# Optimization experiments

Hardware: AMD Instinct MI355X
Metric: run time of the kernel (lower is better)

The kernel has to match this reference:

```python
import jax, jax.numpy as jnp
import numpy as np

EPS = 1e-5

def _conv3x3(x, w, b):
    # NCHW, OIHW, 3x3 stride 1 pad 1
    y = jax.lax.conv_general_dilated(x, w, window_strides=(1, 1),
                                     padding=((1, 1), (1, 1)),
                                     dimension_numbers=('NCHW', 'OIHW', 'NCHW'))
    return y + b[None, :, None, None]

def _pool_upsample(x, k):
    # adaptive avg pool to (H/k, W/k) then nearest block-upsample back
    B, C, H, W = x.shape
    p = x.reshape(B, C, H // k, k, W // k, k).mean(axis=(3, 5))
    return jnp.repeat(jnp.repeat(p, k, axis=2), k, axis=3)

def setup_inputs() -> dict:
    key = jax.random.key(0)
    ks = jax.random.split(key, 12)
    B, C, H, W = 32, 8, 300, 300
    d = {
        'x': jax.random.normal(ks[0], (B, C, H, W), jnp.float32),
        'w5': jax.random.normal(ks[1], (8, 16, 3, 3), jnp.float32) * 0.1,
        'b5': jnp.zeros((8,), jnp.float32),
        'w10': jax.random.normal(ks[2], (8, 16, 3, 3), jnp.float32) * 0.1,
        'b10': jnp.zeros((8,), jnp.float32),
        'w15': jax.random.normal(ks[3], (8, 16, 3, 3), jnp.float32) * 0.1,
        'b15': jnp.zeros((8,), jnp.float32),
        'gw': jax.random.normal(ks[4], (8, 24, 3, 3), jnp.float32) * 0.1,
        'gb': jnp.zeros((8,), jnp.float32),
        'mw': jax.random.normal(ks[5], (8, 24, 3, 3), jnp.float32) * 0.1,
        'mb': jnp.zeros((8,), jnp.float32),
        'gamma': jnp.ones((8,), jnp.float32),
        'beta': jnp.zeros((8,), jnp.float32),
    }
    return d

def reference(x, w5, b5, w10, b10, w15, b15, gw, gb, mw, mb, gamma, beta):
    up5 = _pool_upsample(x, 5)    # [B,8,300,300]
    up10 = _pool_upsample(x, 10)
    up15 = _pool_upsample(x, 15)
    c5 = _conv3x3(jnp.concatenate([x, up5], axis=1), w5, b5)
    c10 = _conv3x3(jnp.concatenate([x, up10], axis=1), w10, b10)
    c15 = _conv3x3(jnp.concatenate([x, up15], axis=1), w15, b15)
    g_in = jnp.concatenate([c5, c10, c15], axis=1)  # [B,24,H,W]
    # gated conv, activation=None: conv(g_in) * sigmoid(mask_conv(g_in))
    y = _conv3x3(g_in, gw, gb) * jax.nn.sigmoid(_conv3x3(g_in, mw, mb))
    # batch norm (training-mode batch stats, biased var, as torch default)
    mean = y.mean(axis=(0, 2, 3), keepdims=True)
    var = ((y - mean) ** 2).mean(axis=(0, 2, 3), keepdims=True)
    y = (y - mean) * jax.lax.rsqrt(var + EPS)
    return y * gamma[None, :, None, None] + beta[None, :, None, None]
```

## Files before the change

### kernel.cpp

```cpp
#include <hip/hip_runtime.h>
#include <math.h>

typedef __bf16 bfrag __attribute__((ext_vector_type(8)));
typedef float f32x4 __attribute__((ext_vector_type(4)));

#define BN 32
#define HH 300
#define WW 300
#define HW 90000
#define NPX (BN * HW)

#define GX 10
#define GY 19

#define P5I_BYTE_OFF   0
#define P10I_BYTE_OFF  1843200
#define P15I_BYTE_OFF  2304000
#define CWB_BYTE_OFF   2508800
#define GWB_BYTE_OFF   2524160
#define STAT_BYTE_OFF  2531328
#define SS_BYTE_OFF    2539520

__device__ __forceinline__ short f2bf(float f) {
    union { float f; unsigned u; } v;
    v.f = f;
    unsigned r = v.u + 0x7FFF + ((v.u >> 16) & 1);
    return (short)(r >> 16);
}

__device__ __forceinline__ float bf2f(unsigned short s) {
    union { unsigned u; float f; } v;
    v.u = ((unsigned)s) << 16;
    return v.f;
}

__global__ void k_setup(const float* __restrict__ w5, const float* __restrict__ w10,
                        const float* __restrict__ w15, const float* __restrict__ gw,
                        const float* __restrict__ mw, short* __restrict__ cBg,
                        short* __restrict__ gBg, double* __restrict__ stats) {
    int t = threadIdx.x;
    for (int idx = t; idx < 7680; idx += 256) {
        int s = idx / 2560, rem = idx % 2560;
        int n = rem / 160, r2 = rem % 160;
        int tap = r2 / 16, ci = r2 % 16;
        float v = 0.f;
        if (n < 8 && tap < 9) {
            const float* W = (s == 0) ? w5 : ((s == 1) ? w10 : w15);
            v = W[(n * 16 + ci) * 9 + tap];
        }
        cBg[idx] = f2bf(v);
    }
    for (int idx = t; idx < 3584; idx += 256) {
        int n = idx / 224, r2 = idx % 224;
        int blk = r2 / 8, cj = r2 % 8;
        float v = 0.f;
        if (blk < 27) {
            int tap = blk / 3, ci24 = (blk % 3) * 8 + cj;
            if (n < 8) v = gw[(n * 24 + ci24) * 9 + tap];
            else       v = mw[((n - 8) * 24 + ci24) * 9 + tap];
        }
        gBg[idx] = f2bf(v);
    }
    for (int idx = t; idx < 16 * 64; idx += 256) stats[idx] = 0.0;
}

__global__ void k_pool5(const float* __restrict__ x, unsigned short* __restrict__ p5i) {
    int id = blockIdx.x * 256 + threadIdx.x;
    int bc = id / 3600, cell = id % 3600;
    int b = bc >> 3, c = bc & 7;
    int pi = cell / 60, pj = cell % 60;
    const float* rp = x + (size_t)bc * HW + pi * 5 * WW + pj * 5;
    float s = 0.f;
#pragma unroll
    for (int u = 0; u < 5; u++)
#pragma unroll
        for (int v = 0; v < 5; v++) s += rp[u * WW + v];
    p5i[((size_t)b * 3600 + cell) * 8 + c] = (unsigned short)f2bf(s * 0.04f);
}

__global__ void k_poolD(const unsigned short* __restrict__ p5i,
                        unsigned short* __restrict__ p10i,
                        unsigned short* __restrict__ p15i) {
    int id = blockIdx.x * 256 + threadIdx.x;
    if (id < 230400) {
        int bc = id / 900, cell = id % 900;
        int b = bc >> 3, c = bc & 7;
        int pi = cell / 30, pj = cell % 30;
        const unsigned short* base = p5i + ((size_t)b * 3600) * 8 + c;
        float s = bf2f(base[((2 * pi) * 60 + 2 * pj) * 8]) +
                  bf2f(base[((2 * pi) * 60 + 2 * pj + 1) * 8]) +
                  bf2f(base[((2 * pi + 1) * 60 + 2 * pj) * 8]) +
                  bf2f(base[((2 * pi + 1) * 60 + 2 * pj + 1) * 8]);
        p10i[((size_t)b * 900 + cell) * 8 + c] = (unsigned short)f2bf(s * 0.25f);
    } else if (id < 332800) {
        int id2 = id - 230400;
        int bc = id2 / 400, cell = id2 % 400;
        int b = bc >> 3, c = bc & 7;
        int pi = cell / 20, pj = cell % 20;
        const unsigned short* base = p5i + ((size_t)b * 3600) * 8 + c;
        float s = 0.f;
#pragma unroll
        for (int u = 0; u < 3; u++)
#pragma unroll
            for (int v = 0; v < 3; v++)
                s += bf2f(base[((3 * pi + u) * 60 + 3 * pj + v) * 8]);
        p15i[((size_t)b * 400 + cell) * 8 + c] = (unsigned short)f2bf(s * (1.f / 9.f));
    }
}

template <int K, int PW>
__device__ __forceinline__ void up_load(const unsigned short* __restrict__ pooled,
                                        int b, int r0, int c0, int t, uint4* v) {
#pragma unroll
    for (int it = 0; it < 3; it++) {
        int idx = t + 256 * it;
        uint4 val = {0u, 0u, 0u, 0u};
        if (idx < 720) {
            int i = idx / 36, j = idx - i * 36;
            int ra = r0 - 2 + i, ca = c0 - 2 + j;
            if (ra >= 0 && ra < HH && ca >= 0 && ca < WW) {
                int pi = (int)((unsigned)ra / K);
                int pj = (int)((unsigned)ca / K);
                val = *(const uint4*)&pooled[((size_t)b * (PW * PW) + pi * PW + pj) * 8];
            }
        }
        v[it] = val;
    }
}

__device__ __forceinline__ void up_store(short* xu, int t, const uint4* v) {
#pragma unroll
    for (int it = 0; it < 3; it++) {
        int idx = t + 256 * it;
        if (idx < 720) *(uint4*)&xu[idx * 16 + 8] = v[it];
    }
}

__device__ __forceinline__ void c_phase(const short* xu, short* cwS,
                                        const unsigned short* __restrict__ cBs,
                                        const float* __restrict__ bias, int s,
                                        int r0, int c0, int lane, int wid) {
    const int n = lane & 15, quad = lane >> 4;
    const int qh = quad >> 1, ql = quad & 1;
    bfrag bfr[5];
    int tapoff[5];
#pragma unroll
    for (int km = 0; km < 5; km++) {
        int tapw = km * 2 + qh;
        int tapa = (tapw > 8) ? 8 : tapw;
        bfr[km] = *(const bfrag*)&cBs[(n * 10 + tapw) * 16 + ql * 8];
        tapoff[km] = ((tapa / 3) * 36 + tapa % 3) * 16;
    }
    float bo = (n < 8) ? bias[n] : 0.f;
    for (int g = wid; g < 39; g += 4) {
        int px = g * 16 + n;
        if (px > 611) px = 611;
        int rp = px / 34, cp = px - rp * 34;
        int off0 = (rp * 36 + cp) * 16 + ql * 8;
        f32x4 acc = {0.f, 0.f, 0.f, 0.f};
#pragma unroll
        for (int km = 0; km < 5; km++)
            acc = __builtin_amdgcn_mfma_f32_16x16x32_bf16(
                *(const bfrag*)&xu[off0 + tapoff[km]], bfr[km], acc, 0, 0, 0);
        if (n < 8) {
            int px2 = g * 16 + quad * 4;
            int r2 = px2 / 34, c2 = px2 - r2 * 34;
#pragma unroll
            for (int reg = 0; reg < 4; reg++) {
                if (px2 + reg < 612) {
                    int ra = r0 - 1 + r2, ca = c0 - 1 + c2;
                    float v = acc[reg] + bo;
                    if (ra < 0 || ra >= HH || ca < 0 || ca >= WW) v = 0.f;
                    cwS[(r2 * 34 + c2) * 24 + s * 8 + n] = f2bf(v);
                }
                c2++;
                if (c2 == 34) { c2 = 0; r2++; }
            }
        }
    }
}

__global__ __launch_bounds__(256, 3) void k_fused(
    const float* __restrict__ x,
    const unsigned short* __restrict__ p5i, const unsigned short* __restrict__ p10i,
    const unsigned short* __restrict__ p15i,
    const unsigned short* __restrict__ cBg, const unsigned short* __restrict__ gBg,
    const float* __restrict__ b5, const float* __restrict__ b10, const float* __restrict__ b15,
    const float* __restrict__ gb, const float* __restrict__ mb,
    float* __restrict__ out, double* __restrict__ stats) {
    __shared__ __align__(16) short xu[20 * 36 * 16];
    __shared__ __align__(16) short cwS[18 * 34 * 24];

    const int b = blockIdx.z;
    const int r0 = blockIdx.y * 16, c0 = blockIdx.x * 32;
    const int t = threadIdx.x, lane = t & 63, wid = t >> 6;

    uint4 upv[3];
    up_load<5, 60>(p5i, b, r0, c0, t, upv);

    for (int idx = t; idx < 1440; idx += 256) {
        int cp = idx / 360, rem = idx % 360;
        int i = rem / 18, jp = rem % 18;
        int j = 2 * jp;
        int ra = r0 - 2 + i, ca = c0 - 2 + j;
        float2 v0 = {0.f, 0.f}, v1 = {0.f, 0.f};
        if (ra >= 0 && ra < HH && ca >= 0 && ca <= WW - 2) {
            size_t base = ((size_t)(b * 8 + 2 * cp) * HH + ra) * WW + ca;
            v0 = *(const float2*)&x[base];
            v1 = *(const float2*)&x[base + HW];
        }
        unsigned pA = (unsigned short)f2bf(v0.x) | ((unsigned)(unsigned short)f2bf(v1.x) << 16);
        unsigned pB = (unsigned short)f2bf(v0.y) | ((unsigned)(unsigned short)f2bf(v1.y) << 16);
        int px = i * 36 + j;
        *(unsigned*)&xu[px * 16 + 2 * cp] = pA;
        *(unsigned*)&xu[(px + 1) * 16 + 2 * cp] = pB;
    }
    up_store(xu, t, upv);
    __syncthreads();

    c_phase(xu, cwS, cBg, b5, 0, r0, c0, lane, wid);
    up_load<10, 30>(p10i, b, r0, c0, t, upv);
    __syncthreads();
    up_store(xu, t, upv);
    __syncthreads();

    c_phase(xu, cwS, cBg + 2560, b10, 1, r0, c0, lane, wid);
    up_load<15, 20>(p15i, b, r0, c0, t, upv);
    __syncthreads();
    up_store(xu, t, upv);
    __syncthreads();

    c_phase(xu, cwS, cBg + 5120, b15, 2, r0, c0, lane, wid);
    __syncthreads();

    const int n = lane & 15, quad = lane >> 4;
    bfrag gfr[7];
    int goff[7];
#pragma unroll
    for (int km = 0; km < 7; km++) {
        int blkw = km * 4 + quad;
        int blka = (blkw > 26) ? 26 : blkw;
        gfr[km] = *(const bfrag*)&gBg[(n * 28 + blkw) * 8];
        int tap = blka / 3, cig = blka - tap * 3;
        goff[km] = ((tap / 3) * 34 + tap % 3) * 24 + cig * 8;
    }
    float gbv = (n < 8) ? gb[n] : 0.f;
    float mbv = (n < 8) ? mb[n] : 0.f;
    float ls = 0.f, ls2 = 0.f;

    for (int g = wid; g < 32; g += 4) {
        int px = g * 16 + n;
        int rr = px >> 5, cc2 = px & 31;
        int off0 = (rr * 34 + cc2) * 24;
        f32x4 acc = {0.f, 0.f, 0.f, 0.f};
#pragma unroll
        for (int km = 0; km < 7; km++)
            acc = __builtin_amdgcn_mfma_f32_16x16x32_bf16(
                *(const bfrag*)&cwS[off0 + goff[km]], gfr[km], acc, 0, 0, 0);
#pragma unroll
        for (int reg = 0; reg < 4; reg++) {
            float other = __shfl_xor(acc[reg], 8);
            if (n < 8) {
                int px2 = g * 16 + quad * 4 + reg;
                int rr2 = px2 >> 5, cc3 = px2 & 31;
                int ra = r0 + rr2, ca = c0 + cc3;
                if (ra < HH && ca < WW) {
                    float G = acc[reg] + gbv, M = other + mbv;
                    float y = G / (1.f + __expf(-M));
                    out[((size_t)(b * 8 + n) * HH + ra) * WW + ca] = y;
                    ls += y;
                    ls2 += y * y;
                }
            }
        }
    }
    ls += __shfl_xor(ls, 16);
    ls += __shfl_xor(ls, 32);
    ls2 += __shfl_xor(ls2, 16);
    ls2 += __shfl_xor(ls2, 32);
    if (lane < 8) {
        int hash = (blockIdx.x + GX * blockIdx.y + GX * GY * blockIdx.z) & 63;
        atomicAdd(&stats[lane * 64 + hash], (double)ls);
        atomicAdd(&stats[(8 + lane) * 64 + hash], (double)ls2);
    }
}

__global__ void k_stats(const double* __restrict__ stats, const float* __restrict__ gamma,
                        const float* __restrict__ beta, float* __restrict__ ss) {
    __shared__ double tot[16];
    int t = threadIdx.x;
    if (t < 16) {
        double s = 0.0;
        for (int i = 0; i < 64; i++) s += stats[t * 64 + i];
        tot[t] = s;
    }
    __syncthreads();
    if (t < 8) {
        double N = (double)NPX;
        double mean = tot[t] / N;
        double var = tot[8 + t] / N - mean * mean;
        double scale = (double)gamma[t] / sqrt(var + 1e-5);
        ss[t] = (float)scale;
        ss[8 + t] = (float)((double)beta[t] - mean * scale);
    }
}

__global__ void k_norm(float* __restrict__ out, const float* __restrict__ ss) {
    int i = blockIdx.x * 256 + threadIdx.x;
    if (i < (BN * 8 * HW) / 4) {
        int plane = (i * 4) / HW;
        int ch = plane & 7;
        float sc = ss[ch], sh = ss[8 + ch];
        float4* p = (float4*)out + i;
        float4 v = *p;
        v.x = v.x * sc + sh;
        v.y = v.y * sc + sh;
        v.z = v.z * sc + sh;
        v.w = v.w * sc + sh;
        *p = v;
    }
}

extern "C" void kernel_launch(void* const* d_in, const int* in_sizes, int n_in,
                              void* d_out, int out_size, void* d_ws, size_t ws_size,
                              hipStream_t stream) {
    const float* x = (const float*)d_in[0];
    const float* w5 = (const float*)d_in[1];
    const float* b5 = (const float*)d_in[2];
    const float* w10 = (const float*)d_in[3];
    const float* b10 = (const float*)d_in[4];
    const float* w15 = (const float*)d_in[5];
    const float* b15 = (const float*)d_in[6];
    const float* gw = (const float*)d_in[7];
    const float* gb = (const float*)d_in[8];
    const float* mw = (const float*)d_in[9];
    const float* mb = (const float*)d_in[10];
    const float* gamma = (const float*)d_in[11];
    const float* beta = (const float*)d_in[12];

    float* out = (float*)d_out;
    unsigned short* p5i = (unsigned short*)((char*)d_ws + P5I_BYTE_OFF);
    unsigned short* p10i = (unsigned short*)((char*)d_ws + P10I_BYTE_OFF);
    unsigned short* p15i = (unsigned short*)((char*)d_ws + P15I_BYTE_OFF);
    short* cBg = (short*)((char*)d_ws + CWB_BYTE_OFF);
    short* gBg = (short*)((char*)d_ws + GWB_BYTE_OFF);
    double* stats = (double*)((char*)d_ws + STAT_BYTE_OFF);
    float* ss = (float*)((char*)d_ws + SS_BYTE_OFF);

    k_setup<<<1, 256, 0, stream>>>(w5, w10, w15, gw, mw, cBg, gBg, stats);
    k_pool5<<<3600, 256, 0, stream>>>(x, p5i);
    k_poolD<<<1300, 256, 0, stream>>>(p5i, p10i, p15i);
    dim3 grid(GX, GY, BN);
    k_fused<<<grid, 256, 0, stream>>>(x, p5i, p10i, p15i,
                                      (const unsigned short*)cBg, (const unsigned short*)gBg,
                                      b5, b10, b15, gb, mb, out, stats);
    k_stats<<<1, 64, 0, stream>>>(stats, gamma, beta, ss);
    k_norm<<<(BN * 8 * HW / 4 + 255) / 256, 256, 0, stream>>>(out, ss);
}
```

Before: 417.7 us.

## Pre-pack input to channel-last bf16 and swap MFMA operands for vectorized epilogues

Adds a prep kernel that converts x to a pixel-major bf16 buffer with 8 channels per pixel, and computes the 5x5 pool in the same pass. The fused kernel can then load each halo pixel with one 16-byte read instead of strided fp32 gathers from 8 channel planes. It also swaps the MFMA A/B operands so each lane holds 4 channels of one pixel, which allows packed bf16x4 stores into shared memory. Edge masking is skipped for interior tiles, and the sigmoid uses a fast reciprocal. The cost is an extra full write and read of a bf16 copy of x, and the new path depends on the workspace being large enough.

```diff
diff --git a/kernel.cpp b/kernel.cpp
--- a/kernel.cpp
+++ b/kernel.cpp
@@ -2,6 +2,8 @@
 #include <math.h>
 
 typedef __bf16 bfrag __attribute__((ext_vector_type(8)));
+typedef __bf16 bf16x4 __attribute__((ext_vector_type(4)));
+typedef __bf16 bf16x8 __attribute__((ext_vector_type(8)));
 typedef float f32x4 __attribute__((ext_vector_type(4)));
 
 #define BN 32
@@ -20,6 +22,8 @@
 #define GWB_BYTE_OFF   2524160
 #define STAT_BYTE_OFF  2531328
 #define SS_BYTE_OFF    2539520
+#define XBF_BYTE_OFF   2539584
+#define XBF_END        (XBF_BYTE_OFF + (size_t)NPX * 16)
 
 __device__ __forceinline__ short f2bf(float f) {
     union { float f; unsigned u; } v;
@@ -76,6 +80,39 @@
 #pragma unroll
         for (int v = 0; v < 5; v++) s += rp[u * WW + v];
     p5i[((size_t)b * 3600 + cell) * 8 + c] = (unsigned short)f2bf(s * 0.04f);
+}
+
+__global__ __launch_bounds__(256) void k_prep(const float* __restrict__ x,
+                                              unsigned short* __restrict__ xbf,
+                                              unsigned short* __restrict__ p5i) {
+    __shared__ float tf[8][5][304];
+    const int t = threadIdx.x;
+    const int pi = blockIdx.x, b = blockIdx.y;
+    for (int idx = t; idx < 3000; idx += 256) {
+        int ch = idx / 375, rem = idx % 375;
+        int r = rem / 75, j = rem % 75;
+        float4 v = *(const float4*)&x[((size_t)(b * 8 + ch) * HH + pi * 5 + r) * WW + 4 * j];
+        *(float4*)&tf[ch][r][4 * j] = v;
+    }
+    __syncthreads();
+    for (int idx = t; idx < 1500; idx += 256) {
+        int r = idx / 300, c = idx - r * 300;
+        bf16x8 pk;
+#pragma unroll
+        for (int ch = 0; ch < 8; ch++) pk[ch] = (__bf16)tf[ch][r][c];
+        *(bf16x8*)&xbf[((size_t)b * HW + (pi * 5 + r) * WW + c) * 8] = pk;
+    }
+    for (int idx = t; idx < 512; idx += 256) {
+        int ch = idx >> 6, pj = idx & 63;
+        if (pj < 60) {
+            float s = 0.f;
+#pragma unroll
+            for (int u = 0; u < 5; u++)
+#pragma unroll
+                for (int v = 0; v < 5; v++) s += tf[ch][u][pj * 5 + v];
+            p5i[((size_t)b * 3600 + pi * 60 + pj) * 8 + ch] = (unsigned short)f2bf(s * 0.04f);
+        }
+    }
 }
 
 __global__ void k_poolD(const unsigned short* __restrict__ p5i,
@@ -128,109 +165,131 @@
     }
 }
 
-__device__ __forceinline__ void up_store(short* xu, int t, const uint4* v) {
+__device__ __forceinline__ void up_store(short* xuU, int t, const uint4* v) {
 #pragma unroll
     for (int it = 0; it < 3; it++) {
         int idx = t + 256 * it;
-        if (idx < 720) *(uint4*)&xu[idx * 16 + 8] = v[it];
-    }
-}
-
-__device__ __forceinline__ void c_phase(const short* xu, short* cwS,
+        if (idx < 720) *(uint4*)&xuU[idx * 8] = v[it];
+    }
+}
+
+__device__ __forceinline__ void c_phase(const short* xuX, const short* xuU,
+                                        short* cwS,
                                         const unsigned short* __restrict__ cBs,
                                         const float* __restrict__ bias, int s,
-                                        int r0, int c0, int lane, int wid) {
+                                        int r0, int c0, int lane, int wid, bool edge) {
     const int n = lane & 15, quad = lane >> 4;
     const int qh = quad >> 1, ql = quad & 1;
-    bfrag bfr[5];
-    int tapoff[5];
+    const short* xbase = ql ? xuU : xuX;
+    bfrag wfr[5];
+    int dpoff[5];
 #pragma unroll
     for (int km = 0; km < 5; km++) {
         int tapw = km * 2 + qh;
         int tapa = (tapw > 8) ? 8 : tapw;
-        bfr[km] = *(const bfrag*)&cBs[(n * 10 + tapw) * 16 + ql * 8];
-        tapoff[km] = ((tapa / 3) * 36 + tapa % 3) * 16;
-    }
-    float bo = (n < 8) ? bias[n] : 0.f;
+        wfr[km] = *(const bfrag*)&cBs[(n * 10 + tapw) * 16 + ql * 8];
+        dpoff[km] = ((tapa / 3) * 36 + tapa % 3) * 8;
+    }
+    float bO[4];
+#pragma unroll
+    for (int r = 0; r < 4; r++) bO[r] = bias[(quad & 1) * 4 + r];
+
     for (int g = wid; g < 39; g += 4) {
         int px = g * 16 + n;
         if (px > 611) px = 611;
-        int rp = px / 34, cp = px - rp * 34;
-        int off0 = (rp * 36 + cp) * 16 + ql * 8;
+        int rp = (int)((unsigned)px / 34u);
+        int cp = px - rp * 34;
+        int pb = (rp * 36 + cp) * 8;
         f32x4 acc = {0.f, 0.f, 0.f, 0.f};
 #pragma unroll
         for (int km = 0; km < 5; km++)
             acc = __builtin_amdgcn_mfma_f32_16x16x32_bf16(
-                *(const bfrag*)&xu[off0 + tapoff[km]], bfr[km], acc, 0, 0, 0);
-        if (n < 8) {
-            int px2 = g * 16 + quad * 4;
-            int r2 = px2 / 34, c2 = px2 - r2 * 34;
-#pragma unroll
-            for (int reg = 0; reg < 4; reg++) {
-                if (px2 + reg < 612) {
-                    int ra = r0 - 1 + r2, ca = c0 - 1 + c2;
-                    float v = acc[reg] + bo;
-                    if (ra < 0 || ra >= HH || ca < 0 || ca >= WW) v = 0.f;
-                    cwS[(r2 * 34 + c2) * 24 + s * 8 + n] = f2bf(v);
+                wfr[km], *(const bfrag*)&xbase[pb + dpoff[km]], acc, 0, 0, 0);
+        if (quad < 2) {
+            bf16x4 pk;
+#pragma unroll
+            for (int r = 0; r < 4; r++) pk[r] = (__bf16)(acc[r] + bO[r]);
+            if (edge) {
+                int ra = r0 - 1 + rp, ca = c0 - 1 + cp;
+                if (ra < 0 || ra >= HH || ca < 0 || ca >= WW) {
+#pragma unroll
+                    for (int r = 0; r < 4; r++) pk[r] = (__bf16)0.f;
                 }
-                c2++;
-                if (c2 == 34) { c2 = 0; r2++; }
             }
-        }
-    }
-}
-
+            *(bf16x4*)&cwS[px * 24 + s * 8 + quad * 4] = pk;
+        }
+    }
+}
+
+template <bool XBF>
 __global__ __launch_bounds__(256, 3) void k_fused(
-    const float* __restrict__ x,
+    const float* __restrict__ x, const unsigned short* __restrict__ xbf,
     const unsigned short* __restrict__ p5i, const unsigned short* __restrict__ p10i,
     const unsigned short* __restrict__ p15i,
     const unsigned short* __restrict__ cBg, const unsigned short* __restrict__ gBg,
     const float* __restrict__ b5, const float* __restrict__ b10, const float* __restrict__ b15,
     const float* __restrict__ gb, const float* __restrict__ mb,
     float* __restrict__ out, double* __restrict__ stats) {
-    __shared__ __align__(16) short xu[20 * 36 * 16];
-    __shared__ __align__(16) short cwS[18 * 34 * 24];
+    __shared__ __align__(16) short xuX[720 * 8];
+    __shared__ __align__(16) short xuU[720 * 8];
+    __shared__ __align__(16) short cwS[612 * 24];
 
     const int b = blockIdx.z;
     const int r0 = blockIdx.y * 16, c0 = blockIdx.x * 32;
     const int t = threadIdx.x, lane = t & 63, wid = t >> 6;
+    const bool edge = (blockIdx.x == 0) | (blockIdx.x == GX - 1) |
+                      (blockIdx.y == 0) | (blockIdx.y == GY - 1);
 
     uint4 upv[3];
     up_load<5, 60>(p5i, b, r0, c0, t, upv);
 
-    for (int idx = t; idx < 1440; idx += 256) {
-        int cp = idx / 360, rem = idx % 360;
-        int i = rem / 18, jp = rem % 18;
-        int j = 2 * jp;
-        int ra = r0 - 2 + i, ca = c0 - 2 + j;
-        float2 v0 = {0.f, 0.f}, v1 = {0.f, 0.f};
-        if (ra >= 0 && ra < HH && ca >= 0 && ca <= WW - 2) {
-            size_t base = ((size_t)(b * 8 + 2 * cp) * HH + ra) * WW + ca;
-            v0 = *(const float2*)&x[base];
-            v1 = *(const float2*)&x[base + HW];
-        }
-        unsigned pA = (unsigned short)f2bf(v0.x) | ((unsigned)(unsigned short)f2bf(v1.x) << 16);
-        unsigned pB = (unsigned short)f2bf(v0.y) | ((unsigned)(unsigned short)f2bf(v1.y) << 16);
-        int px = i * 36 + j;
-        *(unsigned*)&xu[px * 16 + 2 * cp] = pA;
-        *(unsigned*)&xu[(px + 1) * 16 + 2 * cp] = pB;
-    }
-    up_store(xu, t, upv);
-    __syncthreads();
-
-    c_phase(xu, cwS, cBg, b5, 0, r0, c0, lane, wid);
+    if constexpr (XBF) {
+        for (int it = 0; it < 3; it++) {
+            int idx = t + 256 * it;
+            if (idx < 720) {
+                int i = idx / 36, j = idx - i * 36;
+                int ra = r0 - 2 + i, ca = c0 - 2 + j;
+                uint4 v = {0u, 0u, 0u, 0u};
+                if (ra >= 0 && ra < HH && ca >= 0 && ca < WW)
+                    v = *(const uint4*)&xbf[((size_t)b * HW + ra * WW + ca) * 8];
+                *(uint4*)&xuX[idx * 8] = v;
+            }
+        }
+    } else {
+        for (int idx = t; idx < 1440; idx += 256) {
+            int cp = idx / 360, rem = idx % 360;
+            int i = rem / 18, jp = rem % 18;
+            int j = 2 * jp;
+            int ra = r0 - 2 + i, ca = c0 - 2 + j;
+            float2 v0 = {0.f, 0.f}, v1 = {0.f, 0.f};
+            if (ra >= 0 && ra < HH && ca >= 0 && ca <= WW - 2) {
+                size_t base = ((size_t)(b * 8 + 2 * cp) * HH + ra) * WW + ca;
+                v0 = *(const float2*)&x[base];
+                v1 = *(const float2*)&x[base + HW];
+            }
+            unsigned pA = (unsigned short)f2bf(v0.x) | ((unsigned)(unsigned short)f2bf(v1.x) << 16);
+            unsigned pB = (unsigned short)f2bf(v0.y) | ((unsigned)(unsigned short)f2bf(v1.y) << 16);
+            int px = i * 36 + j;
+            *(unsigned*)&xuX[px * 8 + 2 * cp] = pA;
+            *(unsigned*)&xuX[(px + 1) * 8 + 2 * cp] = pB;
+        }
+    }
+    up_store(xuU, t, upv);
+    __syncthreads();
+
+    c_phase(xuX, xuU, cwS, cBg, b5, 0, r0, c0, lane, wid, edge);
     up_load<10, 30>(p10i, b, r0, c0, t, upv);
     __syncthreads();
-    up_store(xu, t, upv);
-    __syncthreads();
-
-    c_phase(xu, cwS, cBg + 2560, b10, 1, r0, c0, lane, wid);
+    up_store(xuU, t, upv);
+    __syncthreads();
+
+    c_phase(xuX, xuU, cwS, cBg + 2560, b10, 1, r0, c0, lane, wid, edge);
     up_load<15, 20>(p15i, b, r0, c0, t, upv);
     __syncthreads();
-    up_store(xu, t, upv);
-    __syncthreads();
-
-    c_phase(xu, cwS, cBg + 5120, b15, 2, r0, c0, lane, wid);
+    up_store(xuU, t, upv);
+    __syncthreads();
+
+    c_phase(xuX, xuU, cwS, cBg + 5120, b15, 2, r0, c0, lane, wid, edge);
     __syncthreads();
 
     const int n = lane & 15, quad = lane >> 4;
@@ -244,44 +303,54 @@
         int tap = blka / 3, cig = blka - tap * 3;
         goff[km] = ((tap / 3) * 34 + tap % 3) * 24 + cig * 8;
     }
-    float gbv = (n < 8) ? gb[n] : 0.f;
-    float mbv = (n < 8) ? mb[n] : 0.f;
-    float ls = 0.f, ls2 = 0.f;
+    float gO[4], mO[4];
+#pragma unroll
+    for (int r = 0; r < 4; r++) {
+        gO[r] = gb[(quad & 1) * 4 + r];
+        mO[r] = mb[(quad & 1) * 4 + r];
+    }
+    float ls[4] = {0.f, 0.f, 0.f, 0.f}, ls2[4] = {0.f, 0.f, 0.f, 0.f};
 
     for (int g = wid; g < 32; g += 4) {
         int px = g * 16 + n;
-        int rr = px >> 5, cc2 = px & 31;
-        int off0 = (rr * 34 + cc2) * 24;
+        int rr = px >> 5, cc = px & 31;
+        int off0 = (rr * 34 + cc) * 24;
         f32x4 acc = {0.f, 0.f, 0.f, 0.f};
 #pragma unroll
         for (int km = 0; km < 7; km++)
             acc = __builtin_amdgcn_mfma_f32_16x16x32_bf16(
-                *(const bfrag*)&cwS[off0 + goff[km]], gfr[km], acc, 0, 0, 0);
+                gfr[km], *(const bfrag*)&cwS[off0 + goff[km]], acc, 0, 0, 0);
+        int ra = r0 + rr, ca = c0 + cc;
+        bool wr = !edge || (ra < HH && ca < WW);
 #pragma unroll
         for (int reg = 0; reg < 4; reg++) {
-            float other = __shfl_xor(acc[reg], 8);
-            if (n < 8) {
-                int px2 = g * 16 + quad * 4 + reg;
-                int rr2 = px2 >> 5, cc3 = px2 & 31;
-                int ra = r0 + rr2, ca = c0 + cc3;
-                if (ra < HH && ca < WW) {
-                    float G = acc[reg] + gbv, M = other + mbv;
-                    float y = G / (1.f + __expf(-M));
-                    out[((size_t)(b * 8 + n) * HH + ra) * WW + ca] = y;
-                    ls += y;
-                    ls2 += y * y;
-                }
+            float other = __shfl_xor(acc[reg], 32);
+            if (quad < 2 && wr) {
+                float G = acc[reg] + gO[reg];
+                float M = other + mO[reg];
+                float y = G * __builtin_amdgcn_rcpf(1.f + __expf(-M));
+                int ch = quad * 4 + reg;
+                out[(size_t)(b * 8 + ch) * HW + ra * WW + ca] = y;
+                ls[reg] += y;
+                ls2[reg] += y * y;
             }
         }
     }
-    ls += __shfl_xor(ls, 16);
-    ls += __shfl_xor(ls, 32);
-    ls2 += __shfl_xor(ls2, 16);
-    ls2 += __shfl_xor(ls2, 32);
-    if (lane < 8) {
+#pragma unroll
+    for (int m = 1; m < 16; m <<= 1) {
+#pragma unroll
+        for (int r = 0; r < 4; r++) {
+            ls[r] += __shfl_xor(ls[r], m);
+            ls2[r] += __shfl_xor(ls2[r], m);
+        }
+    }
+    if (n == 0 && quad < 2) {
         int hash = (blockIdx.x + GX * blockIdx.y + GX * GY * blockIdx.z) & 63;
-        atomicAdd(&stats[lane * 64 + hash], (double)ls);
-        atomicAdd(&stats[(8 + lane) * 64 + hash], (double)ls2);
+#pragma unroll
+        for (int r = 0; r < 4; r++) {
+            atomicAdd(&stats[(quad * 4 + r) * 64 + hash], (double)ls[r]);
+            atomicAdd(&stats[(8 + quad * 4 + r) * 64 + hash], (double)ls2[r]);
+        }
     }
 }
 
@@ -346,14 +415,27 @@
     short* gBg = (short*)((char*)d_ws + GWB_BYTE_OFF);
     double* stats = (double*)((char*)d_ws + STAT_BYTE_OFF);
     float* ss = (float*)((char*)d_ws + SS_BYTE_OFF);
+    unsigned short* xbf = (unsigned short*)((char*)d_ws + XBF_BYTE_OFF);
+
+    const bool use_xbf = (ws_size >= XBF_END);
 
     k_setup<<<1, 256, 0, stream>>>(w5, w10, w15, gw, mw, cBg, gBg, stats);
-    k_pool5<<<3600, 256, 0, stream>>>(x, p5i);
+    if (use_xbf) {
+        k_prep<<<dim3(60, 32), 256, 0, stream>>>(x, xbf, p5i);
+    } else {
+        k_pool5<<<3600, 256, 0, stream>>>(x, p5i);
+    }
     k_poolD<<<1300, 256, 0, stream>>>(p5i, p10i, p15i);
     dim3 grid(GX, GY, BN);
-    k_fused<<<grid, 256, 0, stream>>>(x, p5i, p10i, p15i,
-                                      (const unsigned short*)cBg, (const unsigned short*)gBg,
-                                      b5, b10, b15, gb, mb, out, stats);
+    if (use_xbf) {
+        k_fused<true><<<grid, 256, 0, stream>>>(x, xbf, p5i, p10i, p15i,
+                                                (const unsigned short*)cBg, (const unsigned short*)gBg,
+                                                b5, b10, b15, gb, mb, out, stats);
+    } else {
+        k_fused<false><<<grid, 256, 0, stream>>>(x, xbf, p5i, p10i, p15i,
+                                                 (const unsigned short*)cBg, (const unsigned short*)gBg,
+                                                 b5, b10, b15, gb, mb, out, stats);
+    }
     k_stats<<<1, 64, 0, stream>>>(stats, gamma, beta, ss);
     k_norm<<<(BN * 8 * HW / 4 + 255) / 256, 256, 0, stream>>>(out, ss);
 }
```

Result: faster. 390.7 us (-6.5%).
